# Performance work log

Hardware: AMD Instinct MI355X
Metric: run time of the kernel (lower is better)

Reference implementation:

```python
import jax, jax.numpy as jnp
import numpy as np

DIM = 1024        # model dim
HEADS = 1         # num_heads (fc1 in_features==1 forces this)
HDIM = DIM // HEADS
INNER = 16        # dim_inner
B, L = 2, 4096
ROPE_BASE = 32.0


def _apply_rope(x, pos, base):
    # x: [b, l, h, d]; standard rotate-half RoPE
    d = x.shape[-1]
    inv_freq = base ** (-jnp.arange(0, d, 2, dtype=jnp.float32) / d)   # [d/2]
    ang = pos[:, None].astype(jnp.float32) * inv_freq                  # [l, d/2]
    emb = jnp.concatenate([ang, ang], axis=-1)                         # [l, d]
    cos = jnp.cos(emb)[None, :, None, :].astype(x.dtype)
    sin = jnp.sin(emb)[None, :, None, :].astype(x.dtype)
    x1, x2 = x[..., : d // 2], x[..., d // 2:]
    rot = jnp.concatenate([-x2, x1], axis=-1)
    return x * cos + rot * sin


def setup_inputs() -> dict:
    key = jax.random.key(0)
    ks = jax.random.split(key, 7)
    hidden_states = jax.random.normal(ks[0], (B, L, DIM), dtype=jnp.float32)
    Wq = jax.random.normal(ks[1], (DIM, DIM), dtype=jnp.float32) * 0.02
    Wk = jax.random.normal(ks[2], (DIM, DIM), dtype=jnp.float32) * 0.02
    fc1_w = jax.random.normal(ks[3], (INNER, 1), dtype=jnp.float32) * 0.1
    fc1_b = jax.random.normal(ks[4], (INNER,), dtype=jnp.float32) * 0.1
    fc2_w = jax.random.normal(ks[5], (DIM, INNER), dtype=jnp.float32) * 0.1
    fc2_b = jax.random.normal(ks[6], (DIM,), dtype=jnp.float32) * 0.1
    return {"hidden_states": hidden_states, "Wq": Wq, "Wk": Wk,
            "fc1_w": fc1_w, "fc1_b": fc1_b, "fc2_w": fc2_w, "fc2_b": fc2_b}


def reference(hidden_states, Wq, Wk, fc1_w, fc1_b, fc2_w, fc2_b):
    b, l, _ = hidden_states.shape
    # projections, cast to bf16 as in the torch module
    q = (hidden_states @ Wq.T).reshape(b, l, HEADS, HDIM).astype(jnp.bfloat16)
    k = (hidden_states @ Wk.T).reshape(b, l, HEADS, HDIM).astype(jnp.bfloat16)
    pos = jnp.arange(l)
    q = _apply_rope(q, pos, ROPE_BASE)
    k = _apply_rope(k, pos, ROPE_BASE)
    # causal exp(QK) with NO softmax normalization; accumulate in fp32
    scores = jnp.einsum('bqhd,bkhd->bhqk',
                        q.astype(jnp.float32), k.astype(jnp.float32)) / (HDIM ** 0.5)
    causal = jnp.tril(jnp.ones((l, l), dtype=bool))                    # [l, l]
    exp_qk = jnp.where(causal[None, None], jnp.exp(scores), 0.0)       # [b, h, l, l]
    o = jnp.swapaxes(exp_qk.sum(axis=-1), 1, 2)                        # [b, l, h]
    # small MLP: h(=1) -> INNER -> DIM
    o = jax.nn.relu(o @ fc1_w.T + fc1_b)
    return o @ fc2_w.T + fc2_b                                         # [b, l, DIM]
```

## Files before the change

kernel.cpp:

```cpp
#include <hip/hip_runtime.h>
#include <hip/hip_bf16.h>

typedef __bf16 bf16_t;
typedef __bf16 bf16x4 __attribute__((ext_vector_type(4)));
typedef __bf16 bf16x8 __attribute__((ext_vector_type(8)));
typedef float f32x4 __attribute__((ext_vector_type(4)));

#define B_   2
#define L_   4096
#define DIM_ 1024
#define M_   (B_ * L_)
#define NTASK2_ 272

__device__ __forceinline__ void ld_g2l_16(const bf16_t* g, bf16_t* l) {
  __builtin_amdgcn_global_load_lds(
      (__attribute__((address_space(1))) void*)g,
      (__attribute__((address_space(3))) void*)l, 16, 0, 0);
}

__global__ void cvt_all(const float* __restrict__ hs, const float* __restrict__ wq,
                        const float* __restrict__ wk, bf16_t* __restrict__ hs_b,
                        bf16_t* __restrict__ wq_b, bf16_t* __restrict__ wk_b) {
  const int N_HS = M_ * DIM_ / 4, N_W = DIM_ * DIM_ / 4;
  int i = blockIdx.x * blockDim.x + threadIdx.x;
  const float* s; bf16_t* d; int idx;
  if (i < N_HS)            { s = hs; d = hs_b; idx = i; }
  else if (i < N_HS + N_W) { s = wq; d = wq_b; idx = i - N_HS; }
  else                     { s = wk; d = wk_b; idx = i - N_HS - N_W; }
  float4 v = ((const float4*)s)[idx];
  bf16x4 o = { (bf16_t)v.x, (bf16_t)v.y, (bf16_t)v.z, (bf16_t)v.w };
  ((bf16x4*)d)[idx] = o;
}

__device__ __forceinline__ void core_256x128(const bf16_t* __restrict__ A,
                                             const bf16_t* __restrict__ B,
                                             int K, bf16_t* As, bf16_t* Bs,
                                             f32x4 (&acc)[4][8]) {
  const int tid  = threadIdx.x;
  const int wave = tid >> 6, lane = tid & 63;
  const int quad = lane >> 4, l16 = lane & 15;
  const int srow = lane >> 2;
  const int scol = (((lane & 3) ^ ((lane >> 3) & 3)) * 8);
  const int rsw  = ((l16 >> 1) & 3) * 8;

  for (int kk = 0; kk < K; kk += 32) {
    __syncthreads();
#pragma unroll
    for (int c = 0; c < 6; ++c) {
      int seg = c * 4 + wave;
      if (seg < 16) {
        int row = seg * 16 + srow;
        ld_g2l_16(A + (size_t)row * K + kk + scol, As + seg * 512);
      } else {
        int row = (seg - 16) * 16 + srow;
        ld_g2l_16(B + (size_t)row * K + kk + scol, Bs + (seg - 16) * 512);
      }
    }
    __syncthreads();

    bf16x8 af[4], bfr[8];
#pragma unroll
    for (int i = 0; i < 4; ++i)
      af[i] = *(const bf16x8*)(As + (wave * 64 + i * 16 + l16) * 32 +
                               ((quad * 8) ^ rsw));
#pragma unroll
    for (int j = 0; j < 8; ++j)
      bfr[j] = *(const bf16x8*)(Bs + (j * 16 + l16) * 32 + ((quad * 8) ^ rsw));
#pragma unroll
    for (int i = 0; i < 4; ++i)
#pragma unroll
      for (int j = 0; j < 8; ++j)
        acc[i][j] = __builtin_amdgcn_mfma_f32_16x16x32_bf16(af[i], bfr[j],
                                                            acc[i][j], 0, 0, 0);
  }
}

__global__ __launch_bounds__(256, 2)
void proj_gemm(const bf16_t* __restrict__ A, const bf16_t* __restrict__ Wqb,
               const bf16_t* __restrict__ Wkb, bf16_t* __restrict__ Cq,
               bf16_t* __restrict__ Ck) {
  const int K = DIM_, N = DIM_;
  const bf16_t* Bm = (blockIdx.z == 0) ? Wqb : Wkb;
  bf16_t* Cm = (blockIdx.z == 0) ? Cq : Ck;
  __shared__ __attribute__((aligned(16))) bf16_t As[256 * 32];
  __shared__ __attribute__((aligned(16))) bf16_t Bs[128 * 32];
  const int tid = threadIdx.x;
  const int wave = tid >> 6, lane = tid & 63;
  const int quad = lane >> 4, l16 = lane & 15;
  const int m0 = blockIdx.y * 256, n0 = blockIdx.x * 128;

  f32x4 acc[4][8] = {};
  core_256x128(A + (size_t)m0 * K, Bm + (size_t)n0 * K, K, As, Bs, acc);

#pragma unroll
  for (int i = 0; i < 4; ++i)
#pragma unroll
    for (int j = 0; j < 8; ++j)
#pragma unroll
      for (int r = 0; r < 4; ++r) {
        int m = m0 + wave * 64 + i * 16 + quad * 4 + r;
        int n = n0 + j * 16 + l16;
        Cm[(size_t)m * N + n] = (bf16_t)acc[i][j][r];
      }
}

__global__ void rope_kernel(bf16_t* __restrict__ q, bf16_t* __restrict__ k) {
  bf16_t* x = blockIdx.y ? k : q;
  int row = blockIdx.x * 2 + (threadIdx.x >> 7);
  int j0  = (threadIdx.x & 127) * 4;
  int pos = row & (L_ - 1);
  bf16_t* p = x + (size_t)row * DIM_;
  bf16x4 v1 = *(const bf16x4*)(p + j0);
  bf16x4 v2 = *(const bf16x4*)(p + j0 + 512);
  bf16x4 o1, o2;
#pragma unroll
  for (int u = 0; u < 4; ++u) {
    int j = j0 + u;
    float ang = (float)pos * exp2f((float)j * (-5.0f / 512.0f));
    float c = cosf(ang), s = sinf(ang);
    float cb = (float)(bf16_t)c, sb = (float)(bf16_t)s;
    float x1 = (float)v1[u], x2 = (float)v2[u];
    o1[u] = (bf16_t)(x1 * cb - x2 * sb);
    o2[u] = (bf16_t)(x2 * cb + x1 * sb);
  }
  *(bf16x4*)(p + j0) = o1;
  *(bf16x4*)(p + j0 + 512) = o2;
}

__global__ __launch_bounds__(256, 2)
void attn_rowsum(const bf16_t* __restrict__ Q, const bf16_t* __restrict__ Kc,
                 float* __restrict__ o) {
  int t = blockIdx.x;
  int b = t / NTASK2_;
  t -= b * NTASK2_;
  int mi = (int)((sqrtf(4.0f * (float)t + 1.0f) - 1.0f) * 0.5f);
  while ((mi + 1) * (mi + 2) <= t) ++mi;
  while (mi * (mi + 1) > t) --mi;
  int nt = t - mi * (mi + 1);

  __shared__ __attribute__((aligned(16))) bf16_t As[256 * 32];
  __shared__ __attribute__((aligned(16))) bf16_t Bs[128 * 32];
  const int tid = threadIdx.x;
  const int wave = tid >> 6, lane = tid & 63;
  const int quad = lane >> 4, l16 = lane & 15;

  const bf16_t* A  = Q  + (size_t)b * L_ * DIM_ + (size_t)mi * 256 * DIM_;
  const bf16_t* Bp = Kc + (size_t)b * L_ * DIM_ + (size_t)nt * 128 * DIM_;

  f32x4 acc[4][8] = {};
  core_256x128(A, Bp, DIM_, As, Bs, acc);

  const bool masked = (nt >= 2 * mi);
#pragma unroll
  for (int i = 0; i < 4; ++i) {
#pragma unroll
    for (int r = 0; r < 4; ++r) {
      int grow = mi * 256 + wave * 64 + i * 16 + quad * 4 + r;
      float sum = 0.0f;
#pragma unroll
      for (int j = 0; j < 8; ++j) {
        int gcol = nt * 128 + j * 16 + l16;
        float e = __expf(acc[i][j][r] * 0.03125f);
        if (!masked || gcol <= grow) sum += e;
      }
      sum += __shfl_xor(sum, 1);
      sum += __shfl_xor(sum, 2);
      sum += __shfl_xor(sum, 4);
      sum += __shfl_xor(sum, 8);
      if (l16 == 0)
        atomicAdd(&o[b * L_ + grow], sum);
    }
  }
}

__global__ __launch_bounds__(256)
void mlp_out_kernel(const float* __restrict__ o, const float* __restrict__ fc1_w,
                    const float* __restrict__ fc1_b, const float* __restrict__ fc2_w,
                    const float* __restrict__ fc2_b, float* __restrict__ out) {
  const int R = 16;
  int row0 = blockIdx.x * R;
  int tid = threadIdx.x;
  __shared__ float h[R][16];
  {
    int rl = tid >> 4, i = tid & 15;
    float s = o[row0 + rl];
    h[rl][i] = fmaxf(fc1_w[i] * s + fc1_b[i], 0.0f);
  }
  __syncthreads();
  int d = tid * 4;
  float w[4][16];
#pragma unroll
  for (int c = 0; c < 4; ++c)
#pragma unroll
    for (int i = 0; i < 16; ++i) w[c][i] = fc2_w[(d + c) * 16 + i];
  float4 bb = *(const float4*)(fc2_b + d);
  for (int rl = 0; rl < R; ++rl) {
    float4 v = bb;
#pragma unroll
    for (int i = 0; i < 16; ++i) {
      float hv = h[rl][i];
      v.x += w[0][i] * hv; v.y += w[1][i] * hv;
      v.z += w[2][i] * hv; v.w += w[3][i] * hv;
    }
    *(float4*)(out + (size_t)(row0 + rl) * DIM_ + d) = v;
  }
}

extern "C" void kernel_launch(void* const* d_in, const int* in_sizes, int n_in,
                              void* d_out, int out_size, void* d_ws, size_t ws_size,
                              hipStream_t stream) {
  const float* hs    = (const float*)d_in[0];
  const float* Wq    = (const float*)d_in[1];
  const float* Wk    = (const float*)d_in[2];
  const float* fc1_w = (const float*)d_in[3];
  const float* fc1_b = (const float*)d_in[4];
  const float* fc2_w = (const float*)d_in[5];
  const float* fc2_b = (const float*)d_in[6];
  float* out = (float*)d_out;

  char* ws = (char*)d_ws;
  bf16_t* hs_bf = (bf16_t*)ws; ws += (size_t)M_ * DIM_ * 2;
  bf16_t* wq_bf = (bf16_t*)ws; ws += (size_t)DIM_ * DIM_ * 2;
  bf16_t* wk_bf = (bf16_t*)ws; ws += (size_t)DIM_ * DIM_ * 2;
  bf16_t* q_bf  = (bf16_t*)ws; ws += (size_t)M_ * DIM_ * 2;
  bf16_t* k_bf  = (bf16_t*)ws; ws += (size_t)M_ * DIM_ * 2;
  float*  o     = (float*)ws;

  const int n4 = (M_ * DIM_ + 2 * DIM_ * DIM_) / 4;
  cvt_all<<<n4 / 256, 256, 0, stream>>>(hs, Wq, Wk, hs_bf, wq_bf, wk_bf);

  dim3 gg(DIM_ / 128, M_ / 256, 2);
  proj_gemm<<<gg, 256, 0, stream>>>(hs_bf, wq_bf, wk_bf, q_bf, k_bf);

  dim3 gr(M_ / 2, 2);
  rope_kernel<<<gr, 256, 0, stream>>>(q_bf, k_bf);

  hipMemsetAsync(o, 0, M_ * sizeof(float), stream);
  attn_rowsum<<<B_ * NTASK2_, 256, 0, stream>>>(q_bf, k_bf, o);

  mlp_out_kernel<<<M_ / 16, 256, 0, stream>>>(o, fc1_w, fc1_b, fc2_w, fc2_b, out);
}
```

Before: 242.2 us.

## Triple-buffer async LDS loads with 512x128 tiles and rebalanced causal scheduling

Replaces the synchronous single-buffer GEMM core with a 3-stage global_load_lds pipeline that uses manual vmcnt waits and raw barriers, so loads for step t+2 overlap compute on step t. Tiles grow to 512x128 with 512-thread blocks, and the causal attention grid is remapped to 256 blocks. Diagonal blocks take two tasks each, and waves entirely above the diagonal skip their MFMAs. Larger LDS use (120KB for the three buffers) lowers occupancy, and the hand-written waitcnt logic is fragile.

```diff
diff --git a/kernel.cpp b/kernel.cpp
--- a/kernel.cpp
+++ b/kernel.cpp
@@ -10,7 +10,6 @@
 #define L_   4096
 #define DIM_ 1024
 #define M_   (B_ * L_)
-#define NTASK2_ 272
 
 __device__ __forceinline__ void ld_g2l_16(const bf16_t* g, bf16_t* l) {
   __builtin_amdgcn_global_load_lds(
@@ -32,10 +31,26 @@
   ((bf16x4*)d)[idx] = o;
 }
 
-__device__ __forceinline__ void core_256x128(const bf16_t* __restrict__ A,
-                                             const bf16_t* __restrict__ B,
-                                             int K, bf16_t* As, bf16_t* Bs,
-                                             f32x4 (&acc)[4][8]) {
+#define SEGS_  40
+#define BUFSZ_ (SEGS_ * 512)
+
+__device__ __forceinline__ void stage512(const bf16_t* __restrict__ A,
+                                         const bf16_t* __restrict__ B,
+                                         int kk, bf16_t* buf,
+                                         int wave, int srow, int scol) {
+#pragma unroll
+  for (int c = 0; c < 4; ++c) {
+    int seg = c * 8 + wave;
+    ld_g2l_16(A + (size_t)(seg * 16 + srow) * DIM_ + kk + scol, buf + seg * 512);
+  }
+  ld_g2l_16(B + (size_t)(wave * 16 + srow) * DIM_ + kk + scol,
+            buf + (32 + wave) * 512);
+}
+
+__device__ __forceinline__ void core512(const bf16_t* __restrict__ A,
+                                        const bf16_t* __restrict__ B,
+                                        bf16_t* sm, bool active,
+                                        f32x4 (&acc)[4][8]) {
   const int tid  = threadIdx.x;
   const int wave = tid >> 6, lane = tid & 63;
   const int quad = lane >> 4, l16 = lane & 15;
@@ -43,55 +58,56 @@
   const int scol = (((lane & 3) ^ ((lane >> 3) & 3)) * 8);
   const int rsw  = ((l16 >> 1) & 3) * 8;
 
-  for (int kk = 0; kk < K; kk += 32) {
-    __syncthreads();
-#pragma unroll
-    for (int c = 0; c < 6; ++c) {
-      int seg = c * 4 + wave;
-      if (seg < 16) {
-        int row = seg * 16 + srow;
-        ld_g2l_16(A + (size_t)row * K + kk + scol, As + seg * 512);
-      } else {
-        int row = (seg - 16) * 16 + srow;
-        ld_g2l_16(B + (size_t)row * K + kk + scol, Bs + (seg - 16) * 512);
-      }
+  bf16_t* r0 = sm;
+  bf16_t* r1 = sm + BUFSZ_;
+  bf16_t* r2 = sm + 2 * BUFSZ_;
+
+  stage512(A, B, 0, r0, wave, srow, scol);
+  stage512(A, B, 32, r1, wave, srow, scol);
+
+  for (int t = 0; t < 32; ++t) {
+    if (t < 31) asm volatile("s_waitcnt vmcnt(5)" ::: "memory");
+    else        asm volatile("s_waitcnt vmcnt(0)" ::: "memory");
+    asm volatile("s_barrier" ::: "memory");
+
+    if (t + 2 < 32) stage512(A, B, (t + 2) * 32, r2, wave, srow, scol);
+
+    if (active) {
+      bf16x8 af[4], bfr[8];
+#pragma unroll
+      for (int i = 0; i < 4; ++i)
+        af[i] = *(const bf16x8*)(r0 + (wave * 64 + i * 16 + l16) * 32 +
+                                 ((quad * 8) ^ rsw));
+#pragma unroll
+      for (int j = 0; j < 8; ++j)
+        bfr[j] = *(const bf16x8*)(r0 + 32 * 512 + (j * 16 + l16) * 32 +
+                                  ((quad * 8) ^ rsw));
+#pragma unroll
+      for (int i = 0; i < 4; ++i)
+#pragma unroll
+        for (int j = 0; j < 8; ++j)
+          acc[i][j] = __builtin_amdgcn_mfma_f32_16x16x32_bf16(af[i], bfr[j],
+                                                              acc[i][j], 0, 0, 0);
     }
-    __syncthreads();
-
-    bf16x8 af[4], bfr[8];
-#pragma unroll
-    for (int i = 0; i < 4; ++i)
-      af[i] = *(const bf16x8*)(As + (wave * 64 + i * 16 + l16) * 32 +
-                               ((quad * 8) ^ rsw));
-#pragma unroll
-    for (int j = 0; j < 8; ++j)
-      bfr[j] = *(const bf16x8*)(Bs + (j * 16 + l16) * 32 + ((quad * 8) ^ rsw));
-#pragma unroll
-    for (int i = 0; i < 4; ++i)
-#pragma unroll
-      for (int j = 0; j < 8; ++j)
-        acc[i][j] = __builtin_amdgcn_mfma_f32_16x16x32_bf16(af[i], bfr[j],
-                                                            acc[i][j], 0, 0, 0);
-  }
-}
-
-__global__ __launch_bounds__(256, 2)
+    asm volatile("s_waitcnt lgkmcnt(0)" ::: "memory");
+    bf16_t* tmp = r0; r0 = r1; r1 = r2; r2 = tmp;
+  }
+}
+
+__global__ __launch_bounds__(512, 2)
 void proj_gemm(const bf16_t* __restrict__ A, const bf16_t* __restrict__ Wqb,
                const bf16_t* __restrict__ Wkb, bf16_t* __restrict__ Cq,
                bf16_t* __restrict__ Ck) {
-  const int K = DIM_, N = DIM_;
+  __shared__ __attribute__((aligned(16))) bf16_t sm[3 * BUFSZ_];
   const bf16_t* Bm = (blockIdx.z == 0) ? Wqb : Wkb;
   bf16_t* Cm = (blockIdx.z == 0) ? Cq : Ck;
-  __shared__ __attribute__((aligned(16))) bf16_t As[256 * 32];
-  __shared__ __attribute__((aligned(16))) bf16_t Bs[128 * 32];
-  const int tid = threadIdx.x;
-  const int wave = tid >> 6, lane = tid & 63;
+  const int m0 = blockIdx.y * 512, n0 = blockIdx.x * 128;
+
+  f32x4 acc[4][8] = {};
+  core512(A + (size_t)m0 * DIM_, Bm + (size_t)n0 * DIM_, sm, true, acc);
+
+  const int tid = threadIdx.x, wave = tid >> 6, lane = tid & 63;
   const int quad = lane >> 4, l16 = lane & 15;
-  const int m0 = blockIdx.y * 256, n0 = blockIdx.x * 128;
-
-  f32x4 acc[4][8] = {};
-  core_256x128(A + (size_t)m0 * K, Bm + (size_t)n0 * K, K, As, Bs, acc);
-
 #pragma unroll
   for (int i = 0; i < 4; ++i)
 #pragma unroll
@@ -100,7 +116,7 @@
       for (int r = 0; r < 4; ++r) {
         int m = m0 + wave * 64 + i * 16 + quad * 4 + r;
         int n = n0 + j * 16 + l16;
-        Cm[(size_t)m * N + n] = (bf16_t)acc[i][j][r];
+        Cm[(size_t)m * DIM_ + n] = (bf16_t)acc[i][j][r];
       }
 }
 
@@ -127,48 +143,62 @@
   *(bf16x4*)(p + j0 + 512) = o2;
 }
 
-__global__ __launch_bounds__(256, 2)
+__global__ __launch_bounds__(512, 2)
 void attn_rowsum(const bf16_t* __restrict__ Q, const bf16_t* __restrict__ Kc,
                  float* __restrict__ o) {
-  int t = blockIdx.x;
-  int b = t / NTASK2_;
-  t -= b * NTASK2_;
-  int mi = (int)((sqrtf(4.0f * (float)t + 1.0f) - 1.0f) * 0.5f);
-  while ((mi + 1) * (mi + 2) <= t) ++mi;
-  while (mi * (mi + 1) > t) --mi;
-  int nt = t - mi * (mi + 1);
-
-  __shared__ __attribute__((aligned(16))) bf16_t As[256 * 32];
-  __shared__ __attribute__((aligned(16))) bf16_t Bs[128 * 32];
-  const int tid = threadIdx.x;
-  const int wave = tid >> 6, lane = tid & 63;
+  __shared__ __attribute__((aligned(16))) bf16_t sm[3 * BUFSZ_];
+  const int tid = threadIdx.x, wave = tid >> 6, lane = tid & 63;
   const int quad = lane >> 4, l16 = lane & 15;
 
-  const bf16_t* A  = Q  + (size_t)b * L_ * DIM_ + (size_t)mi * 256 * DIM_;
-  const bf16_t* Bp = Kc + (size_t)b * L_ * DIM_ + (size_t)nt * 128 * DIM_;
-
-  f32x4 acc[4][8] = {};
-  core_256x128(A, Bp, DIM_, As, Bs, acc);
-
-  const bool masked = (nt >= 2 * mi);
-#pragma unroll
-  for (int i = 0; i < 4; ++i) {
-#pragma unroll
-    for (int r = 0; r < 4; ++r) {
-      int grow = mi * 256 + wave * 64 + i * 16 + quad * 4 + r;
-      float sum = 0.0f;
-#pragma unroll
-      for (int j = 0; j < 8; ++j) {
-        int gcol = nt * 128 + j * 16 + l16;
-        float e = __expf(acc[i][j][r] * 0.03125f);
-        if (!masked || gcol <= grow) sum += e;
+  int bid = blockIdx.x;
+  int bb, mi, nt0, nt1, ntasks;
+  if (bid < 224) {
+    bb = bid / 112; int f = bid - bb * 112;
+    int m = 1;
+    while (2 * m * (m + 1) <= f) ++m;
+    mi = m; nt0 = f - 2 * m * (m - 1); nt1 = 0; ntasks = 1;
+  } else if (bid < 240) {
+    int idx = bid - 224; bb = idx >> 3; mi = idx & 7;
+    nt0 = 4 * mi; nt1 = 4 * mi + 3; ntasks = 2;
+  } else {
+    int idx = bid - 240; bb = idx >> 3; mi = idx & 7;
+    nt0 = 4 * mi + 1; nt1 = 4 * mi + 2; ntasks = 2;
+  }
+
+  const bf16_t* Ab = Q  + (size_t)bb * L_ * DIM_ + (size_t)mi * 512 * DIM_;
+  const bf16_t* Kb = Kc + (size_t)bb * L_ * DIM_;
+
+  for (int task = 0; task < ntasks; ++task) {
+    int nt = task ? nt1 : nt0;
+    if (task) __syncthreads();
+
+    bool active = (mi * 512 + wave * 64 + 63) >= nt * 128;
+
+    f32x4 acc[4][8] = {};
+    core512(Ab, Kb + (size_t)nt * 128 * DIM_, sm, active, acc);
+
+    if (active) {
+      const bool masked = (nt >= 4 * mi);
+#pragma unroll
+      for (int i = 0; i < 4; ++i) {
+#pragma unroll
+        for (int r = 0; r < 4; ++r) {
+          int grow = mi * 512 + wave * 64 + i * 16 + quad * 4 + r;
+          float sum = 0.0f;
+#pragma unroll
+          for (int j = 0; j < 8; ++j) {
+            int gcol = nt * 128 + j * 16 + l16;
+            float e = __expf(acc[i][j][r] * 0.03125f);
+            if (!masked || gcol <= grow) sum += e;
+          }
+          sum += __shfl_xor(sum, 1);
+          sum += __shfl_xor(sum, 2);
+          sum += __shfl_xor(sum, 4);
+          sum += __shfl_xor(sum, 8);
+          if (l16 == 0)
+            atomicAdd(&o[bb * L_ + grow], sum);
+        }
       }
-      sum += __shfl_xor(sum, 1);
-      sum += __shfl_xor(sum, 2);
-      sum += __shfl_xor(sum, 4);
-      sum += __shfl_xor(sum, 8);
-      if (l16 == 0)
-        atomicAdd(&o[b * L_ + grow], sum);
     }
   }
 }
@@ -229,14 +259,14 @@
   const int n4 = (M_ * DIM_ + 2 * DIM_ * DIM_) / 4;
   cvt_all<<<n4 / 256, 256, 0, stream>>>(hs, Wq, Wk, hs_bf, wq_bf, wk_bf);
 
-  dim3 gg(DIM_ / 128, M_ / 256, 2);
-  proj_gemm<<<gg, 256, 0, stream>>>(hs_bf, wq_bf, wk_bf, q_bf, k_bf);
+  dim3 gg(DIM_ / 128, M_ / 512, 2);
+  proj_gemm<<<gg, 512, 0, stream>>>(hs_bf, wq_bf, wk_bf, q_bf, k_bf);
 
   dim3 gr(M_ / 2, 2);
   rope_kernel<<<gr, 256, 0, stream>>>(q_bf, k_bf);
 
   hipMemsetAsync(o, 0, M_ * sizeof(float), stream);
-  attn_rowsum<<<B_ * NTASK2_, 256, 0, stream>>>(q_bf, k_bf, o);
+  attn_rowsum<<<256, 512, 0, stream>>>(q_bf, k_bf, o);
 
   mlp_out_kernel<<<M_ / 16, 256, 0, stream>>>(o, fc1_w, fc1_b, fc2_w, fc2_b, out);
 }
```

New measurement: 233.0 us. 3.8% less time.

## Triple-buffer LDS pipeline with 8-wave 2D tiling and causal wave skipping

Applied to the files above, without the earlier changes.

Replaces the two-barrier single-buffer GEMM core with a three-stage LDS ring driven by async global-to-LDS loads, so global fetches for later k-slices overlap MFMA work on the current one. Blocks grow from 4 to 8 waves arranged 4x2, each computing a 64x64 sub-tile. In the attention rowsum, waves whose rows lie entirely above the causal diagonal skip their MFMAs and epilogue. The cost is more LDS per block, explicit waitcnt and barrier bookkeeping, and lower per-wave reuse from the smaller tiles.

```diff
diff --git a/kernel.cpp b/kernel.cpp
--- a/kernel.cpp
+++ b/kernel.cpp
@@ -32,75 +32,100 @@
   ((bf16x4*)d)[idx] = o;
 }
 
-__device__ __forceinline__ void core_256x128(const bf16_t* __restrict__ A,
-                                             const bf16_t* __restrict__ B,
-                                             int K, bf16_t* As, bf16_t* Bs,
-                                             f32x4 (&acc)[4][8]) {
+#define SLICE_SEGS_ 24
+#define BUFSZ_ (SLICE_SEGS_ * 512)
+
+__device__ __forceinline__ void core_256x128_pipe(const bf16_t* __restrict__ A,
+                                                  const bf16_t* __restrict__ B,
+                                                  bf16_t* sm, bool active,
+                                                  f32x4 (&acc)[4][4]) {
   const int tid  = threadIdx.x;
   const int wave = tid >> 6, lane = tid & 63;
+  const int wm = wave >> 1, wn = wave & 1;
   const int quad = lane >> 4, l16 = lane & 15;
   const int srow = lane >> 2;
   const int scol = (((lane & 3) ^ ((lane >> 3) & 3)) * 8);
   const int rsw  = ((l16 >> 1) & 3) * 8;
-
-  for (int kk = 0; kk < K; kk += 32) {
-    __syncthreads();
-#pragma unroll
-    for (int c = 0; c < 6; ++c) {
-      int seg = c * 4 + wave;
-      if (seg < 16) {
-        int row = seg * 16 + srow;
-        ld_g2l_16(A + (size_t)row * K + kk + scol, As + seg * 512);
-      } else {
-        int row = (seg - 16) * 16 + srow;
-        ld_g2l_16(B + (size_t)row * K + kk + scol, Bs + (seg - 16) * 512);
-      }
-    }
-    __syncthreads();
-
-    bf16x8 af[4], bfr[8];
-#pragma unroll
-    for (int i = 0; i < 4; ++i)
-      af[i] = *(const bf16x8*)(As + (wave * 64 + i * 16 + l16) * 32 +
-                               ((quad * 8) ^ rsw));
-#pragma unroll
-    for (int j = 0; j < 8; ++j)
-      bfr[j] = *(const bf16x8*)(Bs + (j * 16 + l16) * 32 + ((quad * 8) ^ rsw));
-#pragma unroll
-    for (int i = 0; i < 4; ++i)
-#pragma unroll
-      for (int j = 0; j < 8; ++j)
-        acc[i][j] = __builtin_amdgcn_mfma_f32_16x16x32_bf16(af[i], bfr[j],
-                                                            acc[i][j], 0, 0, 0);
-  }
-}
-
-__global__ __launch_bounds__(256, 2)
+  const int loff = l16 * 32 + ((quad * 8) ^ rsw);
+
+  const bf16_t* gA0 = A + (size_t)(wave * 16 + srow) * DIM_ + scol;
+  const bf16_t* gA1 = A + (size_t)((wave + 8) * 16 + srow) * DIM_ + scol;
+  const bf16_t* gB  = B + (size_t)(wave * 16 + srow) * DIM_ + scol;
+
+  bf16_t* p0 = sm;
+  bf16_t* p1 = sm + BUFSZ_;
+  bf16_t* p2 = sm + 2 * BUFSZ_;
+
+  ld_g2l_16(gA0,      p0 + wave * 512);
+  ld_g2l_16(gA1,      p0 + (wave + 8) * 512);
+  ld_g2l_16(gB,       p0 + (16 + wave) * 512);
+  ld_g2l_16(gA0 + 32, p1 + wave * 512);
+  ld_g2l_16(gA1 + 32, p1 + (wave + 8) * 512);
+  ld_g2l_16(gB  + 32, p1 + (16 + wave) * 512);
+  gA0 += 64; gA1 += 64; gB += 64;
+  asm volatile("s_waitcnt vmcnt(3)" ::: "memory");
+  __builtin_amdgcn_s_barrier();
+
+  for (int s = 0; s < 32; ++s) {
+    bf16x8 aF[4], bF[4];
+    if (active) {
+#pragma unroll
+      for (int rf = 0; rf < 4; ++rf)
+        aF[rf] = *(const bf16x8*)(p0 + (wm * 4 + rf) * 512 + loff);
+#pragma unroll
+      for (int cf = 0; cf < 4; ++cf)
+        bF[cf] = *(const bf16x8*)(p0 + (16 + wn * 4 + cf) * 512 + loff);
+    }
+    if (s < 30) {
+      ld_g2l_16(gA0, p2 + wave * 512);
+      ld_g2l_16(gA1, p2 + (wave + 8) * 512);
+      ld_g2l_16(gB,  p2 + (16 + wave) * 512);
+      gA0 += 32; gA1 += 32; gB += 32;
+    }
+    __builtin_amdgcn_s_barrier();
+    asm volatile("s_waitcnt lgkmcnt(0)" ::: "memory");
+    __builtin_amdgcn_sched_barrier(0);
+    if (active) {
+      __builtin_amdgcn_s_setprio(1);
+#pragma unroll
+      for (int rf = 0; rf < 4; ++rf)
+#pragma unroll
+        for (int cf = 0; cf < 4; ++cf)
+          acc[rf][cf] = __builtin_amdgcn_mfma_f32_16x16x32_bf16(
+              aF[rf], bF[cf], acc[rf][cf], 0, 0, 0);
+      __builtin_amdgcn_s_setprio(0);
+    }
+    if (s < 30)       asm volatile("s_waitcnt vmcnt(3)" ::: "memory");
+    else if (s == 30) asm volatile("s_waitcnt vmcnt(0)" ::: "memory");
+    __builtin_amdgcn_s_barrier();
+    bf16_t* t0 = p0; p0 = p1; p1 = p2; p2 = t0;
+  }
+}
+
+__global__ __launch_bounds__(512, 2)
 void proj_gemm(const bf16_t* __restrict__ A, const bf16_t* __restrict__ Wqb,
                const bf16_t* __restrict__ Wkb, bf16_t* __restrict__ Cq,
                bf16_t* __restrict__ Ck) {
-  const int K = DIM_, N = DIM_;
+  __shared__ __attribute__((aligned(16))) bf16_t sm[3 * BUFSZ_];
   const bf16_t* Bm = (blockIdx.z == 0) ? Wqb : Wkb;
   bf16_t* Cm = (blockIdx.z == 0) ? Cq : Ck;
-  __shared__ __attribute__((aligned(16))) bf16_t As[256 * 32];
-  __shared__ __attribute__((aligned(16))) bf16_t Bs[128 * 32];
-  const int tid = threadIdx.x;
-  const int wave = tid >> 6, lane = tid & 63;
+  const int m0 = blockIdx.y * 256, n0 = blockIdx.x * 128;
+
+  f32x4 acc[4][4] = {};
+  core_256x128_pipe(A + (size_t)m0 * DIM_, Bm + (size_t)n0 * DIM_, sm, true, acc);
+
+  const int tid = threadIdx.x, wave = tid >> 6, lane = tid & 63;
+  const int wm = wave >> 1, wn = wave & 1;
   const int quad = lane >> 4, l16 = lane & 15;
-  const int m0 = blockIdx.y * 256, n0 = blockIdx.x * 128;
-
-  f32x4 acc[4][8] = {};
-  core_256x128(A + (size_t)m0 * K, Bm + (size_t)n0 * K, K, As, Bs, acc);
-
-#pragma unroll
-  for (int i = 0; i < 4; ++i)
-#pragma unroll
-    for (int j = 0; j < 8; ++j)
+#pragma unroll
+  for (int rf = 0; rf < 4; ++rf)
+#pragma unroll
+    for (int cf = 0; cf < 4; ++cf)
 #pragma unroll
       for (int r = 0; r < 4; ++r) {
-        int m = m0 + wave * 64 + i * 16 + quad * 4 + r;
-        int n = n0 + j * 16 + l16;
-        Cm[(size_t)m * N + n] = (bf16_t)acc[i][j][r];
+        int m = m0 + wm * 64 + rf * 16 + quad * 4 + r;
+        int n = n0 + wn * 64 + cf * 16 + l16;
+        Cm[(size_t)m * DIM_ + n] = (bf16_t)acc[rf][cf][r];
       }
 }
 
@@ -127,9 +152,10 @@
   *(bf16x4*)(p + j0 + 512) = o2;
 }
 
-__global__ __launch_bounds__(256, 2)
+__global__ __launch_bounds__(512, 2)
 void attn_rowsum(const bf16_t* __restrict__ Q, const bf16_t* __restrict__ Kc,
                  float* __restrict__ o) {
+  __shared__ __attribute__((aligned(16))) bf16_t sm[3 * BUFSZ_];
   int t = blockIdx.x;
   int b = t / NTASK2_;
   t -= b * NTASK2_;
@@ -138,37 +164,39 @@
   while (mi * (mi + 1) > t) --mi;
   int nt = t - mi * (mi + 1);
 
-  __shared__ __attribute__((aligned(16))) bf16_t As[256 * 32];
-  __shared__ __attribute__((aligned(16))) bf16_t Bs[128 * 32];
-  const int tid = threadIdx.x;
-  const int wave = tid >> 6, lane = tid & 63;
+  const int tid = threadIdx.x, wave = tid >> 6, lane = tid & 63;
+  const int wm = wave >> 1, wn = wave & 1;
   const int quad = lane >> 4, l16 = lane & 15;
 
   const bf16_t* A  = Q  + (size_t)b * L_ * DIM_ + (size_t)mi * 256 * DIM_;
   const bf16_t* Bp = Kc + (size_t)b * L_ * DIM_ + (size_t)nt * 128 * DIM_;
 
-  f32x4 acc[4][8] = {};
-  core_256x128(A, Bp, DIM_, As, Bs, acc);
-
-  const bool masked = (nt >= 2 * mi);
-#pragma unroll
-  for (int i = 0; i < 4; ++i) {
-#pragma unroll
-    for (int r = 0; r < 4; ++r) {
-      int grow = mi * 256 + wave * 64 + i * 16 + quad * 4 + r;
-      float sum = 0.0f;
-#pragma unroll
-      for (int j = 0; j < 8; ++j) {
-        int gcol = nt * 128 + j * 16 + l16;
-        float e = __expf(acc[i][j][r] * 0.03125f);
-        if (!masked || gcol <= grow) sum += e;
+  bool active = (mi * 256 + wm * 64 + 63) >= nt * 128;
+
+  f32x4 acc[4][4] = {};
+  core_256x128_pipe(A, Bp, sm, active, acc);
+
+  if (active) {
+    const bool masked = (nt >= 2 * mi);
+#pragma unroll
+    for (int rf = 0; rf < 4; ++rf) {
+#pragma unroll
+      for (int r = 0; r < 4; ++r) {
+        int grow = mi * 256 + wm * 64 + rf * 16 + quad * 4 + r;
+        float sum = 0.0f;
+#pragma unroll
+        for (int cf = 0; cf < 4; ++cf) {
+          int gcol = nt * 128 + wn * 64 + cf * 16 + l16;
+          float e = __expf(acc[rf][cf][r] * 0.03125f);
+          if (!masked || gcol <= grow) sum += e;
+        }
+        sum += __shfl_xor(sum, 1);
+        sum += __shfl_xor(sum, 2);
+        sum += __shfl_xor(sum, 4);
+        sum += __shfl_xor(sum, 8);
+        if (l16 == 0)
+          atomicAdd(&o[b * L_ + grow], sum);
       }
-      sum += __shfl_xor(sum, 1);
-      sum += __shfl_xor(sum, 2);
-      sum += __shfl_xor(sum, 4);
-      sum += __shfl_xor(sum, 8);
-      if (l16 == 0)
-        atomicAdd(&o[b * L_ + grow], sum);
     }
   }
 }
@@ -230,13 +258,13 @@
   cvt_all<<<n4 / 256, 256, 0, stream>>>(hs, Wq, Wk, hs_bf, wq_bf, wk_bf);
 
   dim3 gg(DIM_ / 128, M_ / 256, 2);
-  proj_gemm<<<gg, 256, 0, stream>>>(hs_bf, wq_bf, wk_bf, q_bf, k_bf);
+  proj_gemm<<<gg, 512, 0, stream>>>(hs_bf, wq_bf, wk_bf, q_bf, k_bf);
 
   dim3 gr(M_ / 2, 2);
   rope_kernel<<<gr, 256, 0, stream>>>(q_bf, k_bf);
 
   hipMemsetAsync(o, 0, M_ * sizeof(float), stream);
-  attn_rowsum<<<B_ * NTASK2_, 256, 0, stream>>>(q_bf, k_bf, o);
+  attn_rowsum<<<B_ * NTASK2_, 512, 0, stream>>>(q_bf, k_bf, o);
 
   mlp_out_kernel<<<M_ / 16, 256, 0, stream>>>(o, fc1_w, fc1_b, fc2_w, fc2_b, out);
 }
```

After: 229.5 us. -5.2%, faster.
